# Performance work log

Hardware: AMD Instinct MI355X
Metric: run time of the kernel (lower is better)

## Reference

```python
import jax, jax.numpy as jnp
import numpy as np

B, STATE_DIM, T = 4096, 24, 8
V, D, LAT = 65536, 64, 128
NL, NH, MAXDIM, MEM = 3, 8, 32, 10
FF = 4 * LAT  # dim_feedforward = latent_dim * 4 = 512


def setup_inputs():
    key = jax.random.key(0)
    ks = jax.random.split(key, 20)
    w = lambda i, shape, s=0.02: (jax.random.normal(ks[i], shape, jnp.float32) * s)
    return {
        "dimension_tokens": jax.random.randint(ks[0], (STATE_DIM, T), 0, V),
        "dimension_traits": jax.random.normal(ks[1], (B, STATE_DIM, 2), jnp.float32),
        "rel_goal": jax.random.normal(ks[2], (B, STATE_DIM), jnp.float32),
        "memory_context": jax.random.normal(ks[3], (B, MEM, D), jnp.float32),
        "token_embedding": w(4, (V, D), 1.0),
        "dim_embedding": w(5, (MAXDIM, D), 1.0),
        "trait_W": w(6, (D, 2)), "trait_b": jnp.zeros((D,), jnp.float32),
        "intent_W": w(7, (D, 1)), "intent_b": jnp.zeros((D,), jnp.float32),
        "cls_token": w(8, (1, 1, D), 1.0),
        "Wqkv": w(9, (NL, 3 * D, D)), "bqkv": jnp.zeros((NL, 3 * D), jnp.float32),
        "Wo": w(10, (NL, D, D)), "bo": jnp.zeros((NL, D), jnp.float32),
        "ln1_g": jnp.ones((NL, D), jnp.float32), "ln1_b": jnp.zeros((NL, D), jnp.float32),
        "W1": w(11, (NL, FF, D)), "b1": jnp.zeros((NL, FF), jnp.float32),
        "W2": w(12, (NL, D, FF)), "b2": jnp.zeros((NL, D), jnp.float32),
        "ln2_g": jnp.ones((NL, D), jnp.float32), "ln2_b": jnp.zeros((NL, D), jnp.float32),
        "out_W": w(13, (LAT, D)), "out_b": jnp.zeros((LAT,), jnp.float32),
        "out_ln_g": jnp.ones((LAT,), jnp.float32), "out_ln_b": jnp.zeros((LAT,), jnp.float32),
    }


def _ln(x, g, b, eps=1e-5):
    m = jnp.mean(x, -1, keepdims=True)
    v = jnp.var(x, -1, keepdims=True)
    return (x - m) * jax.lax.rsqrt(v + eps) * g + b


def _mha(x, Wqkv, bqkv, Wo, bo):
    Bb, S, Dd = x.shape
    hd = Dd // NH
    qkv = x @ Wqkv.T + bqkv
    q, k, v = jnp.split(qkv, 3, axis=-1)
    heads = lambda t: t.reshape(Bb, S, NH, hd).transpose(0, 2, 1, 3)
    q, k, v = heads(q), heads(k), heads(v)
    scores = jnp.einsum('bhqd,bhkd->bhqk', q, k) * np.float32(1.0 / np.sqrt(hd))
    attn = jax.nn.softmax(scores, axis=-1)
    out = jnp.einsum('bhqk,bhkd->bhqd', attn, v).transpose(0, 2, 1, 3).reshape(Bb, S, Dd)
    return out @ Wo.T + bo


def reference(dimension_tokens, dimension_traits, rel_goal, memory_context,
              token_embedding, dim_embedding, trait_W, trait_b, intent_W, intent_b,
              cls_token, Wqkv, bqkv, Wo, bo, ln1_g, ln1_b, W1, b1, W2, b2,
              ln2_g, ln2_b, out_W, out_b, out_ln_g, out_ln_b):
    Bb = rel_goal.shape[0]
    state_dim = rel_goal.shape[-1]
    # fused gather + mean-pool over each dimension's token list: [state_dim, D]
    tok = jnp.mean(token_embedding[dimension_tokens], axis=1)
    pos = dim_embedding[:state_dim]                                   # [state_dim, D]
    trait_e = dimension_traits @ trait_W.T + trait_b                  # [B, state_dim, D]
    intent_e = rel_goal[..., None] @ intent_W.T + intent_b            # [B, state_dim, D]
    seq = tok[None] + pos[None] + trait_e + intent_e                  # [B, state_dim, D]
    cls = jnp.broadcast_to(cls_token, (Bb, 1, D))
    x = jnp.concatenate([cls, seq, memory_context], axis=1)           # [B, 1+state_dim+MEM, D]
    # post-LN (norm_first=False) TransformerEncoder, dropout=0 (eval)
    for l in range(NL):
        x = _ln(x + _mha(x, Wqkv[l], bqkv[l], Wo[l], bo[l]), ln1_g[l], ln1_b[l])
        ff = jax.nn.gelu(x @ W1[l].T + b1[l], approximate=False) @ W2[l].T + b2[l]
        x = _ln(x + ff, ln2_g[l], ln2_b[l])
    situation = _ln(x[:, 0] @ out_W.T + out_b, out_ln_g, out_ln_b)    # [B, LAT]
    situation_sequence = x[:, 1:1 + state_dim]                        # [B, state_dim, D]
    cur = jnp.mean(situation_sequence, axis=1, keepdims=True)
    new_memory = jnp.concatenate([memory_context, cur], axis=1)[:, -MEM:]
    return situation, situation_sequence, new_memory
```

## Files before the change

### kernel.cpp

```cpp
#include <hip/hip_runtime.h>

typedef _Float16 f16;
typedef _Float16 f16x2 __attribute__((ext_vector_type(2)));
typedef _Float16 f16x4 __attribute__((ext_vector_type(4)));
typedef _Float16 f16x8 __attribute__((ext_vector_type(8)));
typedef float floatx4 __attribute__((ext_vector_type(4)));

#define MFMA(a, b, c) __builtin_amdgcn_mfma_f32_16x16x32_f16((a), (b), (c), 0, 0, 0)

constexpr int S = 35;
constexpr int NH = 8;
constexpr int NL = 3;
constexpr int G = 2;
constexpr int RP = 80;
constexpr int MT = 5;
constexpr int BUF = RP * 64;
constexpr int SEQOFF = 4096 * 128;
constexpr int MEMOFF = SEQOFF + 4096 * 24 * 64;
constexpr int TOKPOS_OFF = 245760;

__device__ __forceinline__ int sw64(int r, int c) {
    return (r << 6) + ((((c >> 3) ^ r) & 7) << 3) + (c & 7);
}
__device__ __forceinline__ int sw128(int r, int c) {
    return (r << 7) + ((((c >> 3) ^ (r & 7))) << 3) + (c & 7);
}

struct Params {
    const int* tok;
    const float *traits, *relg, *mem, *temb, *demb, *traitW, *traitb, *intentW, *intentb, *cls;
    const float *bqkv, *bo, *ln1g, *ln1b, *b1, *b2, *ln2g, *ln2b;
    const float *outW, *outb, *olng, *olnb;
    const f16 *Wqkv, *Wo, *W1, *W2;
    const float* tokpos;
    float* out;
};

__global__ void cvt_all(const float* __restrict__ wqkv, const float* __restrict__ wo,
                        const float* __restrict__ w1, const float* __restrict__ w2,
                        const int* __restrict__ tok, const float* __restrict__ temb,
                        const float* __restrict__ demb, const float* __restrict__ traitb,
                        const float* __restrict__ intentb, f16* __restrict__ dst) {
    if (blockIdx.x == 240) {
        float* tp = (float*)(dst + TOKPOS_OFF);
        for (int idx = threadIdx.x; idx < 24 * 64; idx += 256) {
            int s = idx >> 6, d = idx & 63;
            float a = 0.f;
#pragma unroll
            for (int t = 0; t < 8; ++t) a += temb[tok[s * 8 + t] * 64 + d];
            tp[idx] = a * 0.125f + demb[idx] + traitb[d] + intentb[d];
        }
        return;
    }
    int i = (blockIdx.x * 256 + threadIdx.x) * 4;
    const float* src;
    int off;
    if (i < 36864)       { src = wqkv; off = 0; }
    else if (i < 49152)  { src = wo;   off = 36864; }
    else if (i < 147456) { src = w1;   off = 49152; }
    else                 { src = w2;   off = 147456; }
    floatx4 v = *(const floatx4*)&src[i - off];
    f16x4 o;
    o[0] = (f16)v[0]; o[1] = (f16)v[1]; o[2] = (f16)v[2]; o[3] = (f16)v[3];
    *(f16x4*)&dst[i] = o;
}

__device__ inline f16x4 pack4(float a, float b, float c, float d) {
    f16x2 lo = __builtin_bit_cast(f16x2, __builtin_amdgcn_cvt_pkrtz(a, b));
    f16x2 hi = __builtin_bit_cast(f16x2, __builtin_amdgcn_cvt_pkrtz(c, d));
    f16x4 r; r[0] = lo[0]; r[1] = lo[1]; r[2] = hi[0]; r[3] = hi[1];
    return r;
}

__device__ inline float gelu_f(float x) {
    float x2 = x * x;
    float u = __builtin_fmaf(x2, 0.044715f, 1.0f);
    float xm = x * -2.302585f;
    float z = __builtin_amdgcn_exp2f(xm * u);
    return x * __builtin_amdgcn_rcpf(1.f + z);
}

__device__ inline void ln_row_sw(const f16* buf, f16* dst, int row, const float* g, const float* bb) {
    float v[64];
    float sum = 0.f, sq = 0.f;
#pragma unroll
    for (int kv = 0; kv < 8; ++kv) {
        f16x8 x8 = *(const f16x8*)&buf[sw64(row, kv * 8)];
#pragma unroll
        for (int e = 0; e < 8; ++e) {
            float f = (float)x8[e];
            v[kv * 8 + e] = f;
            sum += f;
            sq += f * f;
        }
    }
    float mean = sum * (1.f / 64.f);
    float var = sq * (1.f / 64.f) - mean * mean;
    float rs = rsqrtf(var + 1e-5f);
#pragma unroll
    for (int kv = 0; kv < 16; ++kv) {
        floatx4 g4 = *(const floatx4*)&g[kv * 4];
        floatx4 b4 = *(const floatx4*)&bb[kv * 4];
        *(f16x4*)&dst[sw64(row, kv * 4)] =
            pack4((v[kv * 4 + 0] - mean) * rs * g4[0] + b4[0],
                  (v[kv * 4 + 1] - mean) * rs * g4[1] + b4[1],
                  (v[kv * 4 + 2] - mean) * rs * g4[2] + b4[2],
                  (v[kv * 4 + 3] - mean) * rs * g4[3] + b4[3]);
    }
}

__global__ __launch_bounds__(256, 4) void fused_tfm_kernel(Params p) {
    __shared__ __align__(16) f16 xlds[BUF];
    __shared__ __align__(16) f16 scratch[3 * BUF];

    f16* qbuf = scratch;
    f16* kbuf = scratch + BUF;
    f16* vbuf = scratch + 2 * BUF;
    f16* hbuf = scratch;

    const int tid = threadIdx.x;
    const int lane = tid & 63;
    const int w = tid >> 6;
    const int l15 = lane & 15;
    const int quad = lane >> 4;
    const int b0 = blockIdx.x * G;

    for (int idx = tid; idx < G * S * 64; idx += 256) {
        int i = idx / (S * 64);
        int rem = idx - i * S * 64;
        int r = rem >> 6, d = rem & 63;
        int b = b0 + i;
        float v;
        if (r == 0) {
            v = p.cls[d];
        } else if (r <= 24) {
            int s = r - 1;
            v = p.tokpos[s * 64 + d] + p.traits[b * 48 + s * 2] * p.traitW[d * 2]
                + p.traits[b * 48 + s * 2 + 1] * p.traitW[d * 2 + 1]
                + p.relg[b * 24 + s] * p.intentW[d];
        } else {
            v = p.mem[b * 640 + (r - 25) * 64 + d];
        }
        xlds[sw64(i * S + r, d)] = (f16)v;
    }
    for (int idx = tid; idx < (RP - G * S) * 64; idx += 256) {
        int r = G * S + (idx >> 6), d = idx & 63;
        xlds[sw64(r, d)] = (f16)0.f;
    }
    __syncthreads();

#pragma unroll 1
    for (int l = 0; l < NL; ++l) {
        const f16* Wqkv_l = p.Wqkv + l * 192 * 64;
        const float* bqkv_l = p.bqkv + l * 192;
        const f16* Wo_l = p.Wo + l * 64 * 64;
        const float* bo_l = p.bo + l * 64;
        const float* ln1g_l = p.ln1g + l * 64;
        const float* ln1b_l = p.ln1b + l * 64;
        const f16* W1_l = p.W1 + l * 512 * 64;
        const float* b1_l = p.b1 + l * 512;
        const f16* W2_l = p.W2 + l * 64 * 512;
        const float* b2_l = p.b2 + l * 64;
        const float* ln2g_l = p.ln2g + l * 64;
        const float* ln2b_l = p.ln2b + l * 64;

        {
            f16x8 xb[MT][2];
#pragma unroll
            for (int m = 0; m < MT; ++m)
#pragma unroll
                for (int kf = 0; kf < 2; ++kf)
                    xb[m][kf] = *(const f16x8*)&xlds[sw64(m * 16 + l15, kf * 32 + quad * 8)];
#pragma unroll
            for (int nt = w; nt < 12; nt += 4) {
                f16x8 wf0 = *(const f16x8*)&Wqkv_l[(nt * 16 + l15) * 64 + quad * 8];
                f16x8 wf1 = *(const f16x8*)&Wqkv_l[(nt * 16 + l15) * 64 + 32 + quad * 8];
                floatx4 bias4 = *(const floatx4*)&bqkv_l[nt * 16 + quad * 4];
                f16* dst = scratch + (nt >> 2) * BUF;
                int oc = (nt & 3) * 16 + quad * 4;
                floatx4 acc[MT];
#pragma unroll
                for (int m = 0; m < MT; ++m) {
                    acc[m] = {0.f, 0.f, 0.f, 0.f};
                    acc[m] = MFMA(wf0, xb[m][0], acc[m]);
                    acc[m] = MFMA(wf1, xb[m][1], acc[m]);
                }
#pragma unroll
                for (int m = 0; m < MT; ++m) {
                    int row = m * 16 + l15;
                    *(f16x4*)&dst[sw64(row, oc)] =
                        pack4(acc[m][0] + bias4[0], acc[m][1] + bias4[1],
                              acc[m][2] + bias4[2], acc[m][3] + bias4[3]);
                }
            }
        }
        __syncthreads();

        for (int t = tid; t < G * NH * S; t += 256) {
            int i = t / (NH * S);
            int rem = t - i * (NH * S);
            int h = rem / S;
            int q = rem - h * S;
            int rbase = i * S;
            const f16x2* qp = (const f16x2*)&qbuf[sw64(rbase + q, h * 8)];
            f16x2 q0 = qp[0], q1 = qp[1], q2 = qp[2], q3 = qp[3];
            float sc[S];
            float mx = -1e30f;
#pragma unroll
            for (int j = 0; j < S; ++j) {
                const f16x2* kp = (const f16x2*)&kbuf[sw64(rbase + j, h * 8)];
                f16x2 acc2 = q0 * kp[0];
                acc2 = q1 * kp[1] + acc2;
                acc2 = q2 * kp[2] + acc2;
                acc2 = q3 * kp[3] + acc2;
                float s = ((float)acc2[0] + (float)acc2[1]) * 0.51006982f;
                sc[j] = s;
                mx = fmaxf(mx, s);
            }
            float lsum = 0.f;
#pragma unroll
            for (int j = 0; j < S; ++j) {
                sc[j] = __builtin_amdgcn_exp2f(sc[j] - mx);
                lsum += sc[j];
            }
            f16x2 o0 = {0.f, 0.f}, o1 = {0.f, 0.f}, o2 = {0.f, 0.f}, o3 = {0.f, 0.f};
#pragma unroll
            for (int j = 0; j < S; ++j) {
                const f16x2* vp = (const f16x2*)&vbuf[sw64(rbase + j, h * 8)];
                f16 sj = (f16)sc[j];
                f16x2 s2 = {sj, sj};
                o0 = vp[0] * s2 + o0;
                o1 = vp[1] * s2 + o1;
                o2 = vp[2] * s2 + o2;
                o3 = vp[3] * s2 + o3;
            }
            f16 invh = (f16)__builtin_amdgcn_rcpf(lsum);
            f16x2 inv2 = {invh, invh};
            o0 *= inv2; o1 *= inv2; o2 *= inv2; o3 *= inv2;
            f16x8 ov;
            ov[0] = o0[0]; ov[1] = o0[1]; ov[2] = o1[0]; ov[3] = o1[1];
            ov[4] = o2[0]; ov[5] = o2[1]; ov[6] = o3[0]; ov[7] = o3[1];
            *(f16x8*)&qbuf[sw64(rbase + q, h * 8)] = ov;
        }
        __syncthreads();

        {
            f16x8 ab[MT][2];
#pragma unroll
            for (int m = 0; m < MT; ++m)
#pragma unroll
                for (int kf = 0; kf < 2; ++kf)
                    ab[m][kf] = *(const f16x8*)&qbuf[sw64(m * 16 + l15, kf * 32 + quad * 8)];
            f16x8 wf0 = *(const f16x8*)&Wo_l[(w * 16 + l15) * 64 + quad * 8];
            f16x8 wf1 = *(const f16x8*)&Wo_l[(w * 16 + l15) * 64 + 32 + quad * 8];
            int oc = w * 16 + quad * 4;
            floatx4 bo4 = *(const floatx4*)&bo_l[oc];
            floatx4 oacc[MT];
#pragma unroll
            for (int m = 0; m < MT; ++m) {
                oacc[m] = {0.f, 0.f, 0.f, 0.f};
                oacc[m] = MFMA(wf0, ab[m][0], oacc[m]);
                oacc[m] = MFMA(wf1, ab[m][1], oacc[m]);
            }
#pragma unroll
            for (int m = 0; m < MT; ++m) {
                int row = m * 16 + l15;
                f16x4 res = *(const f16x4*)&xlds[sw64(row, oc)];
                *(f16x4*)&vbuf[sw64(row, oc)] =
                    pack4(oacc[m][0] + bo4[0] + (float)res[0],
                          oacc[m][1] + bo4[1] + (float)res[1],
                          oacc[m][2] + bo4[2] + (float)res[2],
                          oacc[m][3] + bo4[3] + (float)res[3]);
            }
        }
        __syncthreads();

        if (tid < G * S) ln_row_sw(vbuf, xlds, tid, ln1g_l, ln1b_l);
        __syncthreads();

        {
            f16x8 a2[MT][2];
#pragma unroll
            for (int m = 0; m < MT; ++m)
#pragma unroll
                for (int kf = 0; kf < 2; ++kf)
                    a2[m][kf] = *(const f16x8*)&xlds[sw64(m * 16 + l15, kf * 32 + quad * 8)];
            floatx4 facc[MT];
#pragma unroll
            for (int m = 0; m < MT; ++m) facc[m] = {0.f, 0.f, 0.f, 0.f};

#pragma unroll 1
            for (int c = 0; c < 4; ++c) {
#pragma unroll
                for (int ntl = w; ntl < 8; ntl += 4) {
                    int gc = c * 128 + ntl * 16;
                    f16x8 w1f0 = *(const f16x8*)&W1_l[(gc + l15) * 64 + quad * 8];
                    f16x8 w1f1 = *(const f16x8*)&W1_l[(gc + l15) * 64 + 32 + quad * 8];
                    floatx4 b14 = *(const floatx4*)&b1_l[gc + quad * 4];
                    int oc = ntl * 16 + quad * 4;
                    floatx4 hacc[MT];
#pragma unroll
                    for (int m = 0; m < MT; ++m) {
                        hacc[m] = {0.f, 0.f, 0.f, 0.f};
                        hacc[m] = MFMA(w1f0, a2[m][0], hacc[m]);
                        hacc[m] = MFMA(w1f1, a2[m][1], hacc[m]);
                    }
#pragma unroll
                    for (int m = 0; m < MT; ++m) {
                        int row = m * 16 + l15;
                        *(f16x4*)&hbuf[sw128(row, oc)] =
                            pack4(gelu_f(hacc[m][0] + b14[0]), gelu_f(hacc[m][1] + b14[1]),
                                  gelu_f(hacc[m][2] + b14[2]), gelu_f(hacc[m][3] + b14[3]));
                    }
                }
                __syncthreads();
                f16x8 w2f[4];
#pragma unroll
                for (int kf = 0; kf < 4; ++kf)
                    w2f[kf] = *(const f16x8*)&W2_l[(w * 16 + l15) * 512 + c * 128 + kf * 32 + quad * 8];
#pragma unroll
                for (int m = 0; m < MT; ++m) {
                    f16x8 h0 = *(const f16x8*)&hbuf[sw128(m * 16 + l15, 0 + quad * 8)];
                    f16x8 h1 = *(const f16x8*)&hbuf[sw128(m * 16 + l15, 32 + quad * 8)];
                    f16x8 h2 = *(const f16x8*)&hbuf[sw128(m * 16 + l15, 64 + quad * 8)];
                    f16x8 h3 = *(const f16x8*)&hbuf[sw128(m * 16 + l15, 96 + quad * 8)];
                    facc[m] = MFMA(w2f[0], h0, facc[m]);
                    facc[m] = MFMA(w2f[1], h1, facc[m]);
                    facc[m] = MFMA(w2f[2], h2, facc[m]);
                    facc[m] = MFMA(w2f[3], h3, facc[m]);
                }
                __syncthreads();
            }

            int oc = w * 16 + quad * 4;
            floatx4 b24 = *(const floatx4*)&b2_l[oc];
#pragma unroll
            for (int m = 0; m < MT; ++m) {
                int row = m * 16 + l15;
                f16x4 res = *(const f16x4*)&xlds[sw64(row, oc)];
                *(f16x4*)&vbuf[sw64(row, oc)] =
                    pack4(facc[m][0] + b24[0] + (float)res[0],
                          facc[m][1] + b24[1] + (float)res[1],
                          facc[m][2] + b24[2] + (float)res[2],
                          facc[m][3] + b24[3] + (float)res[3]);
            }
        }
        __syncthreads();

        if (tid < G * S) ln_row_sw(vbuf, xlds, tid, ln2g_l, ln2b_l);
        __syncthreads();
    }

    float* sitlds = (float*)scratch;
    {
        int i = tid >> 7, j = tid & 127;
        float s = p.outb[j];
#pragma unroll
        for (int kv = 0; kv < 8; ++kv) {
            f16x8 xv = *(const f16x8*)&xlds[sw64(i * S, kv * 8)];
            floatx4 w0 = *(const floatx4*)&p.outW[j * 64 + kv * 8];
            floatx4 w1 = *(const floatx4*)&p.outW[j * 64 + kv * 8 + 4];
#pragma unroll
            for (int e = 0; e < 4; ++e) s += (float)xv[e] * w0[e];
#pragma unroll
            for (int e = 0; e < 4; ++e) s += (float)xv[4 + e] * w1[e];
        }
        sitlds[i * 128 + j] = s;
    }
    __syncthreads();

    if (w < 2) {
        int i = w;
        float v0 = sitlds[i * 128 + lane];
        float v1 = sitlds[i * 128 + 64 + lane];
        float sum = v0 + v1, sq = v0 * v0 + v1 * v1;
#pragma unroll
        for (int off = 32; off >= 1; off >>= 1) {
            sum += __shfl_xor(sum, off, 64);
            sq += __shfl_xor(sq, off, 64);
        }
        float mean = sum * (1.f / 128.f);
        float rs = rsqrtf(sq * (1.f / 128.f) - mean * mean + 1e-5f);
        int b = b0 + i;
        __builtin_nontemporal_store((v0 - mean) * rs * p.olng[lane] + p.olnb[lane],
                                    &p.out[b * 128 + lane]);
        __builtin_nontemporal_store((v1 - mean) * rs * p.olng[64 + lane] + p.olnb[64 + lane],
                                    &p.out[b * 128 + 64 + lane]);
    }

    for (int pp = tid; pp < G * 384; pp += 256) {
        int i = pp / 384;
        int q = pp - i * 384;
        int s = q >> 4, dp = (q & 15) * 4;
        int b = b0 + i;
        f16x4 xv = *(const f16x4*)&xlds[sw64(i * S + 1 + s, dp)];
        floatx4 o = {(float)xv[0], (float)xv[1], (float)xv[2], (float)xv[3]};
        __builtin_nontemporal_store(o, (floatx4*)&p.out[SEQOFF + b * 1536 + s * 64 + dp]);
    }
    for (int pp = tid; pp < G * 144; pp += 256) {
        int i = pp / 144;
        int q = pp - i * 144;
        int mr = q >> 4, dp = (q & 15) * 4;
        int b = b0 + i;
        floatx4 v = *(const floatx4*)&p.mem[b * 640 + (1 + mr) * 64 + dp];
        __builtin_nontemporal_store(v, (floatx4*)&p.out[MEMOFF + b * 640 + mr * 64 + dp]);
    }
    if (tid < G * 64) {
        int i = tid >> 6, d = tid & 63;
        float s = 0.f;
#pragma unroll
        for (int sr = 0; sr < 24; ++sr) s += (float)xlds[sw64(i * S + 1 + sr, d)];
        __builtin_nontemporal_store(s * (1.f / 24.f), &p.out[MEMOFF + (b0 + i) * 640 + 576 + d]);
    }
}

extern "C" void kernel_launch(void* const* d_in, const int* in_sizes, int n_in,
                              void* d_out, int out_size, void* d_ws, size_t ws_size,
                              hipStream_t stream) {
    (void)in_sizes; (void)n_in; (void)out_size; (void)ws_size;

    f16* ws = (f16*)d_ws;
    hipLaunchKernelGGL(cvt_all, dim3(241), dim3(256), 0, stream,
                       (const float*)d_in[11], (const float*)d_in[13],
                       (const float*)d_in[17], (const float*)d_in[19],
                       (const int*)d_in[0], (const float*)d_in[4],
                       (const float*)d_in[5], (const float*)d_in[7],
                       (const float*)d_in[9], ws);

    Params p;
    p.tok = (const int*)d_in[0];
    p.traits = (const float*)d_in[1];
    p.relg = (const float*)d_in[2];
    p.mem = (const float*)d_in[3];
    p.temb = (const float*)d_in[4];
    p.demb = (const float*)d_in[5];
    p.traitW = (const float*)d_in[6];
    p.traitb = (const float*)d_in[7];
    p.intentW = (const float*)d_in[8];
    p.intentb = (const float*)d_in[9];
    p.cls = (const float*)d_in[10];
    p.bqkv = (const float*)d_in[12];
    p.bo = (const float*)d_in[14];
    p.ln1g = (const float*)d_in[15];
    p.ln1b = (const float*)d_in[16];
    p.b1 = (const float*)d_in[18];
    p.b2 = (const float*)d_in[20];
    p.ln2g = (const float*)d_in[21];
    p.ln2b = (const float*)d_in[22];
    p.outW = (const float*)d_in[23];
    p.outb = (const float*)d_in[24];
    p.olng = (const float*)d_in[25];
    p.olnb = (const float*)d_in[26];
    p.Wqkv = ws;
    p.Wo = ws + 36864;
    p.W1 = ws + 49152;
    p.W2 = ws + 147456;
    p.tokpos = (const float*)(ws + TOKPOS_OFF);
    p.out = (float*)d_out;

    hipLaunchKernelGGL(fused_tfm_kernel, dim3(4096 / G), dim3(256), 0, stream, p);
}
```

Baseline: 432.8 us.

## Compute attention scores and PV with MFMA using transposed V layout

Replaces the per-thread scalar attention loop with 16x16x16 MFMA for QK^T and PV, one job per (sample, head) per wave, with V written transposed and zero-padded in LDS. The softmax scale is folded into Q at projection time, and the max subtraction is dropped, relying on small score magnitudes. LayerNorm now uses two threads per row with a shuffle reduction. This removes the long serial per-thread dot products but risks overflow without the max subtraction and adds padding work on 35-row tiles.

```diff
diff --git a/kernel.cpp b/kernel.cpp
--- a/kernel.cpp
+++ b/kernel.cpp
@@ -7,6 +7,7 @@
 typedef float floatx4 __attribute__((ext_vector_type(4)));
 
 #define MFMA(a, b, c) __builtin_amdgcn_mfma_f32_16x16x32_f16((a), (b), (c), 0, 0, 0)
+#define MFMA16(a, b, c) __builtin_amdgcn_mfma_f32_16x16x16f16((a), (b), (c), 0, 0, 0)
 
 constexpr int S = 35;
 constexpr int NH = 8;
@@ -18,6 +19,7 @@
 constexpr int SEQOFF = 4096 * 128;
 constexpr int MEMOFF = SEQOFF + 4096 * 24 * 64;
 constexpr int TOKPOS_OFF = 245760;
+constexpr float QSCL = 0.51006982f;
 
 __device__ __forceinline__ int sw64(int r, int c) {
     return (r << 6) + ((((c >> 3) ^ r) & 7) << 3) + (c & 7);
@@ -80,12 +82,14 @@
     return x * __builtin_amdgcn_rcpf(1.f + z);
 }
 
-__device__ inline void ln_row_sw(const f16* buf, f16* dst, int row, const float* g, const float* bb) {
-    float v[64];
+__device__ inline void ln_row_half(const f16* buf, f16* dst, int row, int half,
+                                   const float* g, const float* bb) {
+    float v[32];
     float sum = 0.f, sq = 0.f;
-#pragma unroll
-    for (int kv = 0; kv < 8; ++kv) {
-        f16x8 x8 = *(const f16x8*)&buf[sw64(row, kv * 8)];
+    int c0 = half * 32;
+#pragma unroll
+    for (int kv = 0; kv < 4; ++kv) {
+        f16x8 x8 = *(const f16x8*)&buf[sw64(row, c0 + kv * 8)];
 #pragma unroll
         for (int e = 0; e < 8; ++e) {
             float f = (float)x8[e];
@@ -94,14 +98,16 @@
             sq += f * f;
         }
     }
+    sum += __shfl_xor(sum, 1, 64);
+    sq += __shfl_xor(sq, 1, 64);
     float mean = sum * (1.f / 64.f);
     float var = sq * (1.f / 64.f) - mean * mean;
     float rs = rsqrtf(var + 1e-5f);
 #pragma unroll
-    for (int kv = 0; kv < 16; ++kv) {
-        floatx4 g4 = *(const floatx4*)&g[kv * 4];
-        floatx4 b4 = *(const floatx4*)&bb[kv * 4];
-        *(f16x4*)&dst[sw64(row, kv * 4)] =
+    for (int kv = 0; kv < 8; ++kv) {
+        floatx4 g4 = *(const floatx4*)&g[c0 + kv * 4];
+        floatx4 b4 = *(const floatx4*)&bb[c0 + kv * 4];
+        *(f16x4*)&dst[sw64(row, c0 + kv * 4)] =
             pack4((v[kv * 4 + 0] - mean) * rs * g4[0] + b4[0],
                   (v[kv * 4 + 1] - mean) * rs * g4[1] + b4[1],
                   (v[kv * 4 + 2] - mean) * rs * g4[2] + b4[2],
@@ -176,8 +182,6 @@
                 f16x8 wf0 = *(const f16x8*)&Wqkv_l[(nt * 16 + l15) * 64 + quad * 8];
                 f16x8 wf1 = *(const f16x8*)&Wqkv_l[(nt * 16 + l15) * 64 + 32 + quad * 8];
                 floatx4 bias4 = *(const floatx4*)&bqkv_l[nt * 16 + quad * 4];
-                f16* dst = scratch + (nt >> 2) * BUF;
-                int oc = (nt & 3) * 16 + quad * 4;
                 floatx4 acc[MT];
 #pragma unroll
                 for (int m = 0; m < MT; ++m) {
@@ -185,62 +189,108 @@
                     acc[m] = MFMA(wf0, xb[m][0], acc[m]);
                     acc[m] = MFMA(wf1, xb[m][1], acc[m]);
                 }
-#pragma unroll
-                for (int m = 0; m < MT; ++m) {
-                    int row = m * 16 + l15;
-                    *(f16x4*)&dst[sw64(row, oc)] =
-                        pack4(acc[m][0] + bias4[0], acc[m][1] + bias4[1],
-                              acc[m][2] + bias4[2], acc[m][3] + bias4[3]);
+                if (nt < 4) {
+                    int oc = nt * 16 + quad * 4;
+#pragma unroll
+                    for (int m = 0; m < MT; ++m) {
+                        int row = m * 16 + l15;
+                        *(f16x4*)&qbuf[sw64(row, oc)] =
+                            pack4((acc[m][0] + bias4[0]) * QSCL, (acc[m][1] + bias4[1]) * QSCL,
+                                  (acc[m][2] + bias4[2]) * QSCL, (acc[m][3] + bias4[3]) * QSCL);
+                    }
+                } else if (nt < 8) {
+                    int oc = (nt - 4) * 16 + quad * 4;
+#pragma unroll
+                    for (int m = 0; m < MT; ++m) {
+                        int row = m * 16 + l15;
+                        *(f16x4*)&kbuf[sw64(row, oc)] =
+                            pack4(acc[m][0] + bias4[0], acc[m][1] + bias4[1],
+                                  acc[m][2] + bias4[2], acc[m][3] + bias4[3]);
+                    }
+                } else {
+                    int oc = (nt - 8) * 16 + quad * 4;
+#pragma unroll
+                    for (int m = 0; m < MT; ++m) {
+                        int row = m * 16 + l15;
+                        if (row < 70) {
+                            int ii = row >= 35 ? 1 : 0;
+                            f16* vp = vbuf + ii * 2560 + oc * 40 + (row - ii * 35);
+                            vp[0]   = (f16)(acc[m][0] + bias4[0]);
+                            vp[40]  = (f16)(acc[m][1] + bias4[1]);
+                            vp[80]  = (f16)(acc[m][2] + bias4[2]);
+                            vp[120] = (f16)(acc[m][3] + bias4[3]);
+                        }
+                    }
                 }
             }
+            if (tid < 128) vbuf[(tid >> 6) * 2560 + (tid & 63) * 40 + 35] = (f16)0.f;
         }
         __syncthreads();
 
-        for (int t = tid; t < G * NH * S; t += 256) {
-            int i = t / (NH * S);
-            int rem = t - i * (NH * S);
-            int h = rem / S;
-            int q = rem - h * S;
-            int rbase = i * S;
-            const f16x2* qp = (const f16x2*)&qbuf[sw64(rbase + q, h * 8)];
-            f16x2 q0 = qp[0], q1 = qp[1], q2 = qp[2], q3 = qp[3];
-            float sc[S];
-            float mx = -1e30f;
-#pragma unroll
-            for (int j = 0; j < S; ++j) {
-                const f16x2* kp = (const f16x2*)&kbuf[sw64(rbase + j, h * 8)];
-                f16x2 acc2 = q0 * kp[0];
-                acc2 = q1 * kp[1] + acc2;
-                acc2 = q2 * kp[2] + acc2;
-                acc2 = q3 * kp[3] + acc2;
-                float s = ((float)acc2[0] + (float)acc2[1]) * 0.51006982f;
-                sc[j] = s;
-                mx = fmaxf(mx, s);
+        {
+            f16x4 z4 = {};
+            floatx4 zf = {0.f, 0.f, 0.f, 0.f};
+#pragma unroll 1
+            for (int jj = 0; jj < 4; ++jj) {
+                int job = w * 4 + jj;
+                int i = job >> 3;
+                int h = job & 7;
+                int rbase = i * S;
+                int ccol = h * 8 + (quad & 1) * 4;
+                f16x4 kf[3], vf[3], qf[3];
+#pragma unroll
+                for (int jt = 0; jt < 3; ++jt) {
+                    f16x4 t = *(const f16x4*)&kbuf[sw64(rbase + jt * 16 + l15, ccol)];
+                    kf[jt] = (quad >= 2) ? z4 : t;
+                }
+                const f16* vTb = vbuf + i * 2560 + (h * 8 + (l15 & 7)) * 40;
+                vf[0] = *(const f16x4*)&vTb[quad * 4];
+                vf[1] = *(const f16x4*)&vTb[16 + quad * 4];
+                vf[2] = *(const f16x4*)&vTb[32];
+#pragma unroll
+                for (int qt = 0; qt < 3; ++qt)
+                    qf[qt] = *(const f16x4*)&qbuf[sw64(rbase + qt * 16 + l15, ccol)];
+
+#pragma unroll
+                for (int qt = 0; qt < 3; ++qt) {
+                    floatx4 s0 = MFMA16(kf[0], qf[qt], zf);
+                    floatx4 s1 = MFMA16(kf[1], qf[qt], zf);
+                    floatx4 s2 = MFMA16(kf[2], qf[qt], zf);
+                    float e[12];
+                    float lsum = 0.f;
+#pragma unroll
+                    for (int r = 0; r < 4; ++r) {
+                        e[r] = __builtin_amdgcn_exp2f(s0[r]);
+                        lsum += e[r];
+                    }
+#pragma unroll
+                    for (int r = 0; r < 4; ++r) {
+                        e[4 + r] = __builtin_amdgcn_exp2f(s1[r]);
+                        lsum += e[4 + r];
+                    }
+#pragma unroll
+                    for (int r = 0; r < 4; ++r) {
+                        float v = __builtin_amdgcn_exp2f(s2[r]);
+                        v = (quad == 0 && r < 3) ? v : 0.f;
+                        e[8 + r] = v;
+                        lsum += v;
+                    }
+                    f16x4 p0 = pack4(e[0], e[1], e[2], e[3]);
+                    f16x4 p1 = pack4(e[4], e[5], e[6], e[7]);
+                    f16x4 p2 = pack4(e[8], e[9], e[10], e[11]);
+                    floatx4 acc = {0.f, 0.f, 0.f, 0.f};
+                    acc = MFMA16(vf[0], p0, acc);
+                    acc = MFMA16(vf[1], p1, acc);
+                    acc = MFMA16(vf[2], p2, acc);
+                    lsum += __shfl_xor(lsum, 16, 64);
+                    lsum += __shfl_xor(lsum, 32, 64);
+                    float inv = __builtin_amdgcn_rcpf(lsum);
+                    if (quad < 2 && (qt < 2 || l15 < 3)) {
+                        *(f16x4*)&qbuf[sw64(rbase + qt * 16 + l15, h * 8 + quad * 4)] =
+                            pack4(acc[0] * inv, acc[1] * inv, acc[2] * inv, acc[3] * inv);
+                    }
+                }
             }
-            float lsum = 0.f;
-#pragma unroll
-            for (int j = 0; j < S; ++j) {
-                sc[j] = __builtin_amdgcn_exp2f(sc[j] - mx);
-                lsum += sc[j];
-            }
-            f16x2 o0 = {0.f, 0.f}, o1 = {0.f, 0.f}, o2 = {0.f, 0.f}, o3 = {0.f, 0.f};
-#pragma unroll
-            for (int j = 0; j < S; ++j) {
-                const f16x2* vp = (const f16x2*)&vbuf[sw64(rbase + j, h * 8)];
-                f16 sj = (f16)sc[j];
-                f16x2 s2 = {sj, sj};
-                o0 = vp[0] * s2 + o0;
-                o1 = vp[1] * s2 + o1;
-                o2 = vp[2] * s2 + o2;
-                o3 = vp[3] * s2 + o3;
-            }
-            f16 invh = (f16)__builtin_amdgcn_rcpf(lsum);
-            f16x2 inv2 = {invh, invh};
-            o0 *= inv2; o1 *= inv2; o2 *= inv2; o3 *= inv2;
-            f16x8 ov;
-            ov[0] = o0[0]; ov[1] = o0[1]; ov[2] = o1[0]; ov[3] = o1[1];
-            ov[4] = o2[0]; ov[5] = o2[1]; ov[6] = o3[0]; ov[7] = o3[1];
-            *(f16x8*)&qbuf[sw64(rbase + q, h * 8)] = ov;
         }
         __syncthreads();
 
@@ -275,7 +325,7 @@
         }
         __syncthreads();
 
-        if (tid < G * S) ln_row_sw(vbuf, xlds, tid, ln1g_l, ln1b_l);
+        if (tid < 2 * G * S) ln_row_half(vbuf, xlds, tid >> 1, tid & 1, ln1g_l, ln1b_l);
         __syncthreads();
 
         {
@@ -347,7 +397,7 @@
         }
         __syncthreads();
 
-        if (tid < G * S) ln_row_sw(vbuf, xlds, tid, ln2g_l, ln2b_l);
+        if (tid < 2 * G * S) ln_row_half(vbuf, xlds, tid >> 1, tid & 1, ln2g_l, ln2b_l);
         __syncthreads();
     }
 
```

New measurement: 414.6 us (median of 2 runs). -4.2%, faster.
